# Kernel tuning notes

Measured on AMD Instinct MI355X. Metric: run time of the kernel, lower is better.

## Reference

```python
import jax, jax.numpy as jnp
import numpy as np

EPS = 1e-7  # K.epsilon()

def setup_inputs() -> dict:
    key = jax.random.key(0)
    k1, k2, k3, k4 = jax.random.split(key, 4)
    B, T, D, A = 64, 2048, 256, 128
    x = jax.random.normal(k1, (B, T, D), dtype=jnp.float32)
    # Keras initializers.get('normal') -> RandomNormal(stddev=0.05)
    W = jax.random.normal(k2, (D, A), dtype=jnp.float32) * 0.05
    b = jax.random.normal(k3, (A,), dtype=jnp.float32) * 0.05
    u = jax.random.normal(k4, (A, 1), dtype=jnp.float32) * 0.05
    return {"x": x, "W": W, "b": b, "u": u}

def reference(x, W, b, u):
    # uit = tanh(x @ W + b)  -> [B, T, A]
    uit = jnp.tanh(jnp.einsum('btd,da->bta', x, W) + b)
    # ait = uit @ u, squeeze -> [B, T]
    ait = jnp.einsum('bta,a->bt', uit, u[:, 0])
    ait = jnp.exp(ait)
    # normalize over sequence axis (no mask path)
    ait = ait / (jnp.sum(ait, axis=1, keepdims=True) + EPS)
    # weighted sum pooling over sequence -> [B, D]
    return jnp.einsum('btd,bt->bd', x, ait)
```

## Files before the change

### kernel.cpp

```cpp
#include <hip/hip_runtime.h>

#define BATCH 64
#define TLEN  2048
#define DDIM  256
#define ADIM  128
#define TM    32
#define TILES 4
#define NBLK  (BATCH * TLEN / (TILES * TM))
#define EPSC  1e-7f

typedef __bf16 bf16x8 __attribute__((ext_vector_type(8)));
typedef __bf16 bf16x4 __attribute__((ext_vector_type(4)));
typedef float  f32x4  __attribute__((ext_vector_type(4)));

template <int CTRL>
__device__ __forceinline__ float dpp_add(float v) {
    int vi = __builtin_bit_cast(int, v);
    int sw = __builtin_amdgcn_update_dpp(vi, vi, CTRL, 0xF, 0xF, false);
    return v + __builtin_bit_cast(float, sw);
}

__device__ __forceinline__ void bar_lds() {
    asm volatile("s_waitcnt lgkmcnt(0)" ::: "memory");
    __builtin_amdgcn_s_barrier();
}


__global__ __launch_bounds__(256, 2) void attn_main(const float* __restrict__ x,
                                                    const float* __restrict__ W,
                                                    const float* __restrict__ bias,
                                                    const float* __restrict__ u,
                                                    float* __restrict__ Npart,
                                                    float* __restrict__ spart) {
    __shared__ char  xs[TM * DDIM * 2];
    __shared__ float wpart[4][TM];
    __shared__ float fpart[4][32][8];
    __shared__ float ssum_lds[4];

    const int bid  = blockIdx.x;
    const int b    = bid >> 4;
    const int t00  = (bid & 15) * (TILES * TM);
    const int tid  = threadIdx.x;
    const int wave = tid >> 6;
    const int lane = tid & 63;
    const int lm   = lane & 15;
    const int lk   = lane >> 4;

    const float* xw = x + ((size_t)(b * TLEN + t00) + wave * 8) * DDIM;

    f32x4 fa[8];
#pragma unroll
    for (int i = 0; i < 8; ++i)
        fa[i] = *(const f32x4*)(xw + i * DDIM + lane * 4);

    bf16x8 wfreg[8][2];
#pragma unroll
    for (int kt = 0; kt < 8; ++kt)
#pragma unroll
        for (int ntl = 0; ntl < 2; ++ntl) {
            const float* wp = W + (size_t)(kt * 32 + lk * 8) * ADIM + wave * 32 + ntl * 16 + lm;
            bf16x8 w;
#pragma unroll
            for (int j = 0; j < 8; ++j) w[j] = (__bf16)wp[j * ADIM];
            wfreg[kt][ntl] = w;
        }

    float bias_r[2], u_r[2];
#pragma unroll
    for (int ntl = 0; ntl < 2; ++ntl) {
        bias_r[ntl] = bias[wave * 32 + ntl * 16 + lm];
        u_r[ntl]    = u[wave * 32 + ntl * 16 + lm];
    }

    float vacc[8] = {0.f, 0.f, 0.f, 0.f, 0.f, 0.f, 0.f, 0.f};
    float sreg = 0.f;
    const int dgrp = tid & 31;
    const int tgrp = tid >> 5;

    for (int it = 0; it < TILES; ++it) {
#pragma unroll
        for (int i = 0; i < 8; ++i) {
            const int row = wave * 8 + i;
            bf16x4 a;
#pragma unroll
            for (int j = 0; j < 4; ++j) a[j] = (__bf16)fa[i][j];
            *(bf16x4*)(xs + ((row * 512 + lane * 8) ^ (i << 4))) = a;
        }
        if (it + 1 < TILES) {
            const float* xn = xw + (size_t)(it + 1) * TM * DDIM;
#pragma unroll
            for (int i = 0; i < 8; ++i)
                fa[i] = *(const f32x4*)(xn + i * DDIM + lane * 4);
        }
        bar_lds();

        f32x4 acc[2][2];
#pragma unroll
        for (int m = 0; m < 2; ++m)
#pragma unroll
            for (int ntl = 0; ntl < 2; ++ntl) acc[m][ntl] = (f32x4){0.f, 0.f, 0.f, 0.f};

#pragma unroll
        for (int kt = 0; kt < 8; ++kt) {
#pragma unroll
            for (int m = 0; m < 2; ++m) {
                const int r = m * 16 + lm;
                bf16x8 afrag = *(const bf16x8*)(xs + ((r * 512 + kt * 64 + lk * 16) ^ ((r & 7) << 4)));
                acc[m][0] = __builtin_amdgcn_mfma_f32_16x16x32_bf16(afrag, wfreg[kt][0], acc[m][0], 0, 0, 0);
                acc[m][1] = __builtin_amdgcn_mfma_f32_16x16x32_bf16(afrag, wfreg[kt][1], acc[m][1], 0, 0, 0);
            }
        }

#pragma unroll
        for (int m = 0; m < 2; ++m) {
#pragma unroll
            for (int reg = 0; reg < 4; ++reg) {
                float p = 0.f;
#pragma unroll
                for (int ntl = 0; ntl < 2; ++ntl) {
                    float lg = acc[m][ntl][reg] + bias_r[ntl];
                    float e  = __expf(2.0f * lg);
                    float th = 1.0f - 2.0f * __builtin_amdgcn_rcpf(e + 1.0f);
                    p += th * u_r[ntl];
                }
                p = dpp_add<0xB1>(p);
                p = dpp_add<0x4E>(p);
                p = dpp_add<0x141>(p);
                p = dpp_add<0x140>(p);
                if (lm == 0) wpart[wave][m * 16 + lk * 4 + reg] = p;
            }
        }
        bar_lds();

        f32x4 z = (f32x4){0.f, 0.f, 0.f, 0.f};
#pragma unroll
        for (int w = 0; w < 4; ++w) z += *(const f32x4*)&wpart[w][tgrp * 4];
        float wv[4];
#pragma unroll
        for (int i = 0; i < 4; ++i) { wv[i] = __expf(z[i]); sreg += wv[i]; }

#pragma unroll
        for (int i = 0; i < 4; ++i) {
            const int t = tgrp * 4 + i;
            bf16x8 xv = *(const bf16x8*)(xs + ((t * 512 + dgrp * 16) ^ ((t & 7) << 4)));
#pragma unroll
            for (int j = 0; j < 8; ++j) vacc[j] += (float)xv[j] * wv[i];
        }
        bar_lds();
    }

    float ss = sreg;
#pragma unroll
    for (int off = 1; off < 64; off <<= 1) ss += __shfl_xor(ss, off);
    if (lane == 0) ssum_lds[wave] = ss;

#pragma unroll
    for (int j = 0; j < 8; ++j) vacc[j] += __shfl_xor(vacc[j], 32);
    if (lane < 32) {
        *(f32x4*)&fpart[wave][dgrp][0] = (f32x4){vacc[0], vacc[1], vacc[2], vacc[3]};
        *(f32x4*)&fpart[wave][dgrp][4] = (f32x4){vacc[4], vacc[5], vacc[6], vacc[7]};
    }
    __syncthreads();
    if (tid == 0)
        spart[bid] = (ssum_lds[0] + ssum_lds[1] + ssum_lds[2] + ssum_lds[3]) * (1.0f / 32.0f);
    Npart[(size_t)bid * DDIM + tid] =
          fpart[0][tid >> 3][tid & 7] + fpart[1][tid >> 3][tid & 7]
        + fpart[2][tid >> 3][tid & 7] + fpart[3][tid >> 3][tid & 7];
}

__global__ __launch_bounds__(256) void finalize_kernel(const float* __restrict__ Npart,
                                                       const float* __restrict__ spart,
                                                       float* __restrict__ out) {
    const int b = blockIdx.x;
    const int d = threadIdx.x;
    float sb = 0.f;
#pragma unroll
    for (int i = 0; i < 16; ++i) sb += spart[b * 16 + i];
    float r = 0.f;
#pragma unroll
    for (int i = 0; i < 16; ++i) r += Npart[(size_t)(b * 16 + i) * DDIM + d];
    out[b * DDIM + d] = r / (sb + EPSC);
}

extern "C" void kernel_launch(void* const* d_in, const int* in_sizes, int n_in,
                              void* d_out, int out_size, void* d_ws, size_t ws_size,
                              hipStream_t stream) {
    const float* x    = (const float*)d_in[0];
    const float* W    = (const float*)d_in[1];
    const float* bias = (const float*)d_in[2];
    const float* u    = (const float*)d_in[3];
    float* out = (float*)d_out;

    char* ws = (char*)d_ws;
    float* Npart = (float*)ws;
    float* spart = (float*)(ws + 1048576);

    attn_main<<<NBLK, 256, 0, stream>>>(x, W, bias, u, Npart, spart);
    finalize_kernel<<<BATCH, 256, 0, stream>>>(Npart, spart, out);
}
```

Before: 35.00 us.

## Fuse finalize into main kernel via last-block atomic counter, double-buffer LDS

Removes the separate finalize kernel launch by having each block publish its partials and increment a per-batch atomic counter; the last block of each batch reduces the 16 partials and writes the output. The LDS x tile is double-buffered so the trailing barrier of each tile iteration can be dropped. This adds a memset launch for the counters, plus atomic traffic and a serialized tail reduction done in the final block of each batch.

```diff
diff --git a/kernel.cpp b/kernel.cpp
--- a/kernel.cpp
+++ b/kernel.cpp
@@ -31,11 +31,14 @@
                                                     const float* __restrict__ bias,
                                                     const float* __restrict__ u,
                                                     float* __restrict__ Npart,
-                                                    float* __restrict__ spart) {
-    __shared__ char  xs[TM * DDIM * 2];
+                                                    float* __restrict__ spart,
+                                                    int* __restrict__ cnt,
+                                                    float* __restrict__ out) {
+    __shared__ char  xs[2][TM * DDIM * 2];
     __shared__ float wpart[4][TM];
     __shared__ float fpart[4][32][8];
     __shared__ float ssum_lds[4];
+    __shared__ int   done_lds;
 
     const int bid  = blockIdx.x;
     const int b    = bid >> 4;
@@ -78,13 +81,14 @@
     const int tgrp = tid >> 5;
 
     for (int it = 0; it < TILES; ++it) {
+        char* buf = xs[it & 1];
 #pragma unroll
         for (int i = 0; i < 8; ++i) {
             const int row = wave * 8 + i;
             bf16x4 a;
 #pragma unroll
             for (int j = 0; j < 4; ++j) a[j] = (__bf16)fa[i][j];
-            *(bf16x4*)(xs + ((row * 512 + lane * 8) ^ (i << 4))) = a;
+            *(bf16x4*)(buf + ((row * 512 + lane * 8) ^ (i << 4))) = a;
         }
         if (it + 1 < TILES) {
             const float* xn = xw + (size_t)(it + 1) * TM * DDIM;
@@ -105,7 +109,7 @@
 #pragma unroll
             for (int m = 0; m < 2; ++m) {
                 const int r = m * 16 + lm;
-                bf16x8 afrag = *(const bf16x8*)(xs + ((r * 512 + kt * 64 + lk * 16) ^ ((r & 7) << 4)));
+                bf16x8 afrag = *(const bf16x8*)(buf + ((r * 512 + kt * 64 + lk * 16) ^ ((r & 7) << 4)));
                 acc[m][0] = __builtin_amdgcn_mfma_f32_16x16x32_bf16(afrag, wfreg[kt][0], acc[m][0], 0, 0, 0);
                 acc[m][1] = __builtin_amdgcn_mfma_f32_16x16x32_bf16(afrag, wfreg[kt][1], acc[m][1], 0, 0, 0);
             }
@@ -142,11 +146,10 @@
 #pragma unroll
         for (int i = 0; i < 4; ++i) {
             const int t = tgrp * 4 + i;
-            bf16x8 xv = *(const bf16x8*)(xs + ((t * 512 + dgrp * 16) ^ ((t & 7) << 4)));
+            bf16x8 xv = *(const bf16x8*)(buf + ((t * 512 + dgrp * 16) ^ ((t & 7) << 4)));
 #pragma unroll
             for (int j = 0; j < 8; ++j) vacc[j] += (float)xv[j] * wv[i];
         }
-        bar_lds();
     }
 
     float ss = sreg;
@@ -161,25 +164,37 @@
         *(f32x4*)&fpart[wave][dgrp][4] = (f32x4){vacc[4], vacc[5], vacc[6], vacc[7]};
     }
     __syncthreads();
-    if (tid == 0)
-        spart[bid] = (ssum_lds[0] + ssum_lds[1] + ssum_lds[2] + ssum_lds[3]) * (1.0f / 32.0f);
-    Npart[(size_t)bid * DDIM + tid] =
-          fpart[0][tid >> 3][tid & 7] + fpart[1][tid >> 3][tid & 7]
-        + fpart[2][tid >> 3][tid & 7] + fpart[3][tid >> 3][tid & 7];
-}
-
-__global__ __launch_bounds__(256) void finalize_kernel(const float* __restrict__ Npart,
-                                                       const float* __restrict__ spart,
-                                                       float* __restrict__ out) {
-    const int b = blockIdx.x;
-    const int d = threadIdx.x;
-    float sb = 0.f;
-#pragma unroll
-    for (int i = 0; i < 16; ++i) sb += spart[b * 16 + i];
-    float r = 0.f;
-#pragma unroll
-    for (int i = 0; i < 16; ++i) r += Npart[(size_t)(b * 16 + i) * DDIM + d];
-    out[b * DDIM + d] = r / (sb + EPSC);
+
+    float r = fpart[0][tid >> 3][tid & 7] + fpart[1][tid >> 3][tid & 7]
+            + fpart[2][tid >> 3][tid & 7] + fpart[3][tid >> 3][tid & 7];
+    __hip_atomic_store(&Npart[(size_t)bid * DDIM + tid], r,
+                       __ATOMIC_RELAXED, __HIP_MEMORY_SCOPE_AGENT);
+    if (tid == 0) {
+        float sblock = (ssum_lds[0] + ssum_lds[1] + ssum_lds[2] + ssum_lds[3]) * (1.0f / 32.0f);
+        __hip_atomic_store(&spart[bid], sblock,
+                           __ATOMIC_RELAXED, __HIP_MEMORY_SCOPE_AGENT);
+    }
+    __syncthreads();
+
+    if (tid == 0) {
+        int old = __hip_atomic_fetch_add(&cnt[b], 1,
+                                         __ATOMIC_ACQ_REL, __HIP_MEMORY_SCOPE_AGENT);
+        done_lds = (old == 15);
+    }
+    __syncthreads();
+    if (done_lds) {
+        float sb = 0.f;
+#pragma unroll
+        for (int i = 0; i < 16; ++i)
+            sb += __hip_atomic_load(&spart[b * 16 + i],
+                                    __ATOMIC_RELAXED, __HIP_MEMORY_SCOPE_AGENT);
+        float nv = 0.f;
+#pragma unroll
+        for (int i = 0; i < 16; ++i)
+            nv += __hip_atomic_load(&Npart[(size_t)(b * 16 + i) * DDIM + tid],
+                                    __ATOMIC_RELAXED, __HIP_MEMORY_SCOPE_AGENT);
+        out[b * DDIM + tid] = nv / (sb + EPSC);
+    }
 }
 
 extern "C" void kernel_launch(void* const* d_in, const int* in_sizes, int n_in,
@@ -194,7 +209,8 @@
     char* ws = (char*)d_ws;
     float* Npart = (float*)ws;
     float* spart = (float*)(ws + 1048576);
-
-    attn_main<<<NBLK, 256, 0, stream>>>(x, W, bias, u, Npart, spart);
-    finalize_kernel<<<BATCH, 256, 0, stream>>>(Npart, spart, out);
-}
+    int*   cnt   = (int*)(ws + 1052672);
+
+    hipMemsetAsync(cnt, 0, 256, stream);
+    attn_main<<<NBLK, 256, 0, stream>>>(x, W, bias, u, Npart, spart, cnt, out);
+}
```

New measurement: 63.12 us. +80.3%, slower.
